# Kernel tuning notes

Measured on AMD Instinct MI355X. Metric: run time of the kernel, lower is better.

Reference implementation:

```python
import jax, jax.numpy as jnp
import numpy as np

N, E, IN_DIM, OUT_DIM, R = 50000, 800000, 128, 128, 8


def setup_inputs() -> dict:
    key = jax.random.key(0)
    k1, k2, k3, k4, k5 = jax.random.split(key, 5)
    x = jax.random.normal(k1, (N, IN_DIM), dtype=jnp.float32)
    edge_index = jax.random.randint(k2, (2, E), 0, N, dtype=jnp.int32)
    edge_type = jax.random.randint(k3, (E,), 0, R, dtype=jnp.int32)
    # Xavier-uniform-ish init for parameters
    lim_w = float(np.sqrt(6.0 / (IN_DIM + OUT_DIM)))
    weight = jax.random.uniform(k4, (R, IN_DIM, OUT_DIM), dtype=jnp.float32, minval=-lim_w, maxval=lim_w)
    self_weight = jax.random.uniform(k5, (IN_DIM, OUT_DIM), dtype=jnp.float32, minval=-lim_w, maxval=lim_w)
    return {"x": x, "weight": weight, "self_weight": self_weight,
            "edge_index": edge_index, "edge_type": edge_type}


def reference(x, weight, self_weight, edge_index, edge_type):
    n = x.shape[0]
    r = weight.shape[0]
    d_out = weight.shape[2]
    src, dst = edge_index[0], edge_index[1]
    # undirected: symmetrize edges (directed=False)
    src_all = jnp.concatenate([src, dst])          # [2E]
    dst_all = jnp.concatenate([dst, src])          # [2E]
    et_all = jnp.concatenate([edge_type, edge_type])  # [2E]
    # transform all nodes by every relation weight once: [R, N, D_out]
    xw = jnp.einsum('ni,rio->rno', x, weight)
    # gather per-edge messages already transformed by their relation's W_r
    msg = xw[et_all, src_all]                      # [2E, D_out]
    # fused (relation, dst) segment id -> per-relation scatter-add
    seg = et_all.astype(jnp.int32) * n + dst_all
    agg = jax.ops.segment_sum(msg, seg, num_segments=r * n).reshape(r, n, d_out)
    deg = jax.ops.segment_sum(jnp.ones_like(seg, dtype=x.dtype), seg,
                              num_segments=r * n).reshape(r, n)
    deg_inv = jnp.where(deg > 0, 1.0 / jnp.maximum(deg, 1.0), jnp.zeros_like(deg))
    out = jnp.sum(agg * deg_inv[..., None], axis=0)  # [N, D_out]
    out = out + x @ self_weight                       # self-loop
    return out
```

## Files before the change

kernel.cpp:

```cpp
#include <hip/hip_runtime.h>

#define NN 50000
#define EE 800000
#define RR 8
#define DD 128
#define SS (NN*RR)
#define TE (2*EE)
#define NB 782
#define NBLK 391
#define NS (NB*NBLK)
#define CONVB 6826
#define XWB 391

typedef __attribute__((ext_vector_type(8))) short bf16x8;
typedef __attribute__((ext_vector_type(4))) float f32x4;

#define DRAIN_VM do { \
    asm volatile("s_waitcnt vmcnt(0)" ::: "memory"); \
    __builtin_amdgcn_sched_barrier(0); \
  } while (0)

__device__ __forceinline__ unsigned short f2bf(float f){
  unsigned int u = __float_as_uint(f);
  u += 0x7fffu + ((u >> 16) & 1u);
  return (unsigned short)(u >> 16);
}
__device__ __forceinline__ float bf_lo(unsigned int w){ return __uint_as_float(w << 16); }
__device__ __forceinline__ float bf_hi(unsigned int w){ return __uint_as_float(w & 0xffff0000u); }

__device__ __forceinline__ void acc8(float* a, uint4 u){
  a[0] += bf_lo(u.x); a[1] += bf_hi(u.x);
  a[2] += bf_lo(u.y); a[3] += bf_hi(u.y);
  a[4] += bf_lo(u.z); a[5] += bf_hi(u.z);
  a[6] += bf_lo(u.w); a[7] += bf_hi(u.w);
}
__device__ __forceinline__ void acc8s(float* a, uint4 u, float s){
  a[0] += s*bf_lo(u.x); a[1] += s*bf_hi(u.x);
  a[2] += s*bf_lo(u.y); a[3] += s*bf_hi(u.y);
  a[4] += s*bf_lo(u.z); a[5] += s*bf_hi(u.z);
  a[6] += s*bf_lo(u.w); a[7] += s*bf_hi(u.w);
}

__device__ __forceinline__ void dir_edge(const int* ei, const int* et, int j,
                                         int& s, int& d, int& t){
  if (j < EE){ s = ei[j]; d = ei[EE + j]; t = et[j]; }
  else { int jj = j - EE; s = ei[EE + jj]; d = ei[jj]; t = et[jj]; }
}

__global__ __launch_bounds__(256) void k_histconv(
    const int* __restrict__ ei, const int* __restrict__ et,
    int* __restrict__ hist,
    const float* __restrict__ x, const float* __restrict__ w,
    const float* __restrict__ sw,
    unsigned short* __restrict__ xb, unsigned short* __restrict__ wb)
{
  __shared__ int h[NB];
  if (blockIdx.x < NBLK){
    int tid = threadIdx.x, bid = blockIdx.x;
    for (int i = tid; i < NB; i += 256) h[i] = 0;
    __syncthreads();
    int j0 = bid*4096;
    for (int k = tid; k < 4096; k += 256){
      int j = j0 + k;
      if (j < TE){
        int s, d, t; dir_edge(ei, et, j, s, d, t);
        atomicAdd(&h[d >> 6], 1);
      }
    }
    __syncthreads();
    for (int i = tid; i < NB; i += 256) hist[i*NBLK + bid] = h[i];
  } else {
    int i = (blockIdx.x - NBLK)*256 + threadIdx.x;
    const int M1 = NN*DD/4;
    if (i < M1){
      float4 v = ((const float4*)x)[i];
      ushort4 o;
      o.x = f2bf(v.x); o.y = f2bf(v.y); o.z = f2bf(v.z); o.w = f2bf(v.w);
      ((ushort4*)xb)[i] = o;
    } else {
      int j = i - M1;
      if (j < 9*DD*DD){
        int r = j >> 14; int rem = j & 16383; int n = rem >> 7; int k = rem & 127;
        float v = (r < 8) ? w[r*16384 + k*128 + n] : sw[k*128 + n];
        wb[j] = f2bf(v);
      }
    }
  }
}

__global__ __launch_bounds__(256) void k_scan1(int* __restrict__ hist,
                                               int* __restrict__ blksum){
  __shared__ int sd[256];
  int b = blockIdx.x, tid = threadIdx.x;
  int base = b*1024 + tid*4;
  int v0 = (base+0 < NS) ? hist[base+0] : 0;
  int v1 = (base+1 < NS) ? hist[base+1] : 0;
  int v2 = (base+2 < NS) ? hist[base+2] : 0;
  int v3 = (base+3 < NS) ? hist[base+3] : 0;
  int ts = v0+v1+v2+v3;
  sd[tid] = ts; __syncthreads();
  for (int o = 1; o < 256; o <<= 1){
    int t = (tid >= o) ? sd[tid-o] : 0;
    __syncthreads();
    sd[tid] += t;
    __syncthreads();
  }
  int ex = sd[tid] - ts;
  if (base+0 < NS) hist[base+0] = ex; ex += v0;
  if (base+1 < NS) hist[base+1] = ex; ex += v1;
  if (base+2 < NS) hist[base+2] = ex; ex += v2;
  if (base+3 < NS) hist[base+3] = ex;
  if (tid == 255) blksum[b] = sd[255];
}

__global__ __launch_bounds__(256) void k_scan3(int* __restrict__ hist,
                                               const int* __restrict__ blksum){
  __shared__ int sd[256];
  int b = blockIdx.x, tid = threadIdx.x;
  int chunk = b >> 2;
  int s = 0;
  if (tid < chunk)       s  = blksum[tid];
  if (tid + 256 < chunk) s += blksum[tid + 256];
  sd[tid] = s; __syncthreads();
  for (int o = 128; o > 0; o >>= 1){
    if (tid < o) sd[tid] += sd[tid + o];
    __syncthreads();
  }
  int i = b*256 + tid;
  if (i < NS) hist[i] += sd[0];
}

__global__ __launch_bounds__(256, 5) void k_partxw(
    const int* __restrict__ ei, const int* __restrict__ et,
    const int* __restrict__ S, unsigned int* __restrict__ P,
    const unsigned short* __restrict__ xb,
    const unsigned short* __restrict__ wb,
    unsigned short* __restrict__ xw)
{
  __shared__ __align__(16) unsigned short Bs[2][4096];
  if (blockIdx.x < NBLK){
    int* cur = (int*)&Bs[0][0];
    int tid = threadIdx.x, bid = blockIdx.x;
    for (int i = tid; i < NB; i += 256) cur[i] = S[i*NBLK + bid];
    __syncthreads();
    int j0 = bid*4096;
    for (int k = tid; k < 4096; k += 256){
      int j = j0 + k;
      if (j < TE){
        int s, d, t; dir_edge(ei, et, j, s, d, t);
        int b = d >> 6;
        int p = atomicAdd(&cur[b], 1);
        P[p] = (unsigned int)s | ((unsigned int)(d & 63) << 17)
             | ((unsigned int)t << 23);
      }
    }
  } else {
    const int bid  = blockIdx.x - NBLK;
    const int tid  = threadIdx.x;
    const int wave = tid >> 6, lane = tid & 63;
    const int l15  = lane & 15, quad = lane >> 4;
    const int row0 = bid * 128 + wave * 32;

    bf16x8 af[2][4];
    #pragma unroll
    for (int m = 0; m < 2; ++m){
      int gr = row0 + m*16 + l15; if (gr >= NN) gr = NN - 1;
      #pragma unroll
      for (int ks = 0; ks < 4; ++ks)
        af[m][ks] = *(const bf16x8*)(xb + (size_t)gr*DD + ks*32 + quad*8);
    }

    auto stage = [&](int rr, int qq, int bfb){
      #pragma unroll
      for (int j = 0; j < 2; ++j){
        int rowq = (wave*2 + j)*4 + (lane >> 4);
        int n = qq*32 + rowq;
        int c = lane & 15;
        const unsigned short* gp = wb + rr*16384 + n*128 + ((c ^ (n & 7)) << 3);
        __builtin_amdgcn_global_load_lds(
            (const __attribute__((address_space(1))) void*)gp,
            (__attribute__((address_space(3))) void*)((char*)&Bs[bfb][0] + (wave*2 + j)*1024),
            16, 0, 0);
      }
    };

    stage(0, 0, 0);

    #pragma unroll 1
    for (int r = 0; r < 9; ++r){
      unsigned short* xs = xw + (size_t)r * NN * DD;
      #pragma unroll
      for (int q = 0; q < 4; ++q){
        DRAIN_VM;
        __syncthreads();
        {
          int nqq = r*4 + q + 1;
          if (nqq < 36) stage(nqq >> 2, nqq & 3, (q + 1) & 1);
        }
        const char* bb = (const char*)&Bs[q & 1][0];
        #pragma unroll
        for (int lnt = 0; lnt < 2; ++lnt){
          int nt = q*2 + lnt;
          bf16x8 bf4[4];
          #pragma unroll
          for (int ks = 0; ks < 4; ++ks)
            bf4[ks] = *(const bf16x8*)(bb + (lnt*16 + l15)*256
                                          + (((ks*4 + quad) ^ (l15 & 7)) << 4));
          f32x4 C0 = (f32x4)(0.f), C1 = (f32x4)(0.f);
          #pragma unroll
          for (int ks = 0; ks < 4; ++ks){
            C0 = __builtin_amdgcn_mfma_f32_16x16x32_bf16(af[0][ks], bf4[ks], C0, 0, 0, 0);
            C1 = __builtin_amdgcn_mfma_f32_16x16x32_bf16(af[1][ks], bf4[ks], C1, 0, 0, 0);
          }
          #pragma unroll
          for (int i = 0; i < 4; ++i){
            int gr0 = row0 + quad*4 + i;
            int gr1 = row0 + 16 + quad*4 + i;
            if (gr0 < NN) xs[(size_t)gr0*DD + nt*16 + l15] = f2bf(C0[i]);
            if (gr1 < NN) xs[(size_t)gr1*DD + nt*16 + l15] = f2bf(C1[i]);
          }
        }
      }
    }
  }
}

__global__ __launch_bounds__(256) void k_build(const unsigned int* __restrict__ P,
                                               const int* __restrict__ S,
                                               int* __restrict__ esrc,
                                               int* __restrict__ offs){
  __shared__ int h[512], cu[512], sd[256];
  int tid = threadIdx.x, b = blockIdx.x;
  int pstart = S[b*NBLK];
  int pend   = (b+1 < NB) ? S[(b+1)*NBLK] : TE;
  int ne = pend - pstart;
  h[2*tid] = 0; h[2*tid+1] = 0;
  __syncthreads();
  for (int k = tid; k < ne; k += 256){
    unsigned int u = P[pstart + k];
    int lseg = (int)(((u >> 17) & 63u)*8u + (u >> 23));
    atomicAdd(&h[lseg], 1);
  }
  __syncthreads();
  int v0 = h[2*tid], v1 = h[2*tid+1];
  int ts = v0 + v1;
  sd[tid] = ts; __syncthreads();
  for (int o = 1; o < 256; o <<= 1){
    int t = (tid >= o) ? sd[tid-o] : 0;
    __syncthreads();
    sd[tid] += t;
    __syncthreads();
  }
  int ex = sd[tid] - ts;
  cu[2*tid]   = pstart + ex;
  cu[2*tid+1] = pstart + ex + v0;
  int seg0 = b*512;
  if (seg0 + 2*tid     < SS) offs[seg0 + 2*tid]     = cu[2*tid];
  if (seg0 + 2*tid + 1 < SS) offs[seg0 + 2*tid + 1] = cu[2*tid+1];
  if (b == NB-1 && tid == 0) offs[SS] = TE;
  __syncthreads();
  for (int k = tid; k < ne; k += 256){
    unsigned int u = P[pstart + k];
    int lseg = (int)(((u >> 17) & 63u)*8u + (u >> 23));
    int r = atomicAdd(&cu[lseg], 1);
    esrc[r] = (int)(u & 0x1ffffu) | (int)(((u >> 23) & 7u) << 17);
  }
}

__global__ __launch_bounds__(256, 4) void k_agg(
    const unsigned short* __restrict__ xw,
    const int* __restrict__ offs,
    const int* __restrict__ esrc,
    float* __restrict__ out)
{
  const int tid   = threadIdx.x;
  const int lane  = tid & 63;
  const int gl    = lane & 15;
  const int basel = lane & 48;
  const int d     = blockIdx.x * 16 + (tid >> 4);

  int o = 0;
  if (gl < 9) o = offs[d*8 + gl];
  int onx = __shfl(o, (basel + gl + 1) & 63);
  int cnt = onx - o;
  float scale = (gl < 8 && cnt > 0) ? 1.0f/(float)cnt : 0.0f;
  int ebase = __shfl(o, basel);
  int etot  = __shfl(o, basel + 8) - ebase;

  float a[8] = {0.f,0.f,0.f,0.f,0.f,0.f,0.f,0.f};

  int pk[8];
  #pragma unroll
  for (int s = 0; s < 8; ++s) pk[s] = (s < etot) ? esrc[ebase + s] : 0;

  for (int e = 0; e < etot; e += 8){
    uint4 U[8]; float sc[8];
    #pragma unroll
    for (int s = 0; s < 8; ++s){
      sc[s] = 0.f;
      U[s] = make_uint4(0u,0u,0u,0u);
      if (e + s < etot){
        int rel = (pk[s] >> 17) & 7;
        sc[s]   = __shfl(scale, basel + rel);
        int src = pk[s] & 0x1ffff;
        U[s] = *(const uint4*)(xw + ((size_t)rel*NN + src)*DD + gl*8);
      }
    }
    #pragma unroll
    for (int s = 0; s < 8; ++s){
      int en = e + 8 + s;
      pk[s] = (en < etot) ? esrc[ebase + en] : 0;
    }
    #pragma unroll
    for (int s = 0; s < 8; ++s) acc8s(a, U[s], sc[s]);
  }

  {
    uint4 u = *(const uint4*)(xw + ((size_t)8*NN + d)*DD + gl*8);
    acc8(a, u);
  }

  float4 v0; v0.x = a[0]; v0.y = a[1]; v0.z = a[2]; v0.w = a[3];
  float4 v1; v1.x = a[4]; v1.y = a[5]; v1.z = a[6]; v1.w = a[7];
  *(float4*)(out + (size_t)d*DD + gl*8)     = v0;
  *(float4*)(out + (size_t)d*DD + gl*8 + 4) = v1;
}

extern "C" void kernel_launch(void* const* d_in, const int* in_sizes, int n_in,
                              void* d_out, int out_size, void* d_ws, size_t ws_size,
                              hipStream_t stream){
  const float* x  = (const float*)d_in[0];
  const float* w  = (const float*)d_in[1];
  const float* sw = (const float*)d_in[2];
  const int*   ei = (const int*)d_in[3];
  const int*   et = (const int*)d_in[4];
  float* out = (float*)d_out;
  char* ws = (char*)d_ws;

  if (ws_size < (size_t)136295168) return;

  unsigned short* xb = (unsigned short*)(ws + 0);
  int*          esrc = (int*)(ws + 12800000);
  int*          offs = (int*)(ws + 19200000);
  unsigned short* wb = (unsigned short*)(ws + 20800016);
  unsigned short* xw = (unsigned short*)(ws + 21095168);

  unsigned int*    P = (unsigned int*)((char*)d_out + 0);
  int*          hist = (int*)((char*)d_out + 6400000);
  int*        blksum = (int*)((char*)d_out + 7623168);

  k_histconv<<<NBLK + CONVB, 256, 0, stream>>>(ei, et, hist, x, w, sw, xb, wb);
  k_scan1<<<(NS + 1023)/1024, 256, 0, stream>>>(hist, blksum);
  k_scan3<<<(NS + 255)/256, 256, 0, stream>>>(hist, blksum);
  k_partxw<<<NBLK + XWB, 256, 0, stream>>>(ei, et, hist, P, xb, wb, xw);
  k_build<<<NB, 256, 0, stream>>>(P, hist, esrc, offs);
  k_agg<<<NN/16, 256, 0, stream>>>(xw, offs, esrc, out);
}
```

Baseline: 229.4 us.

## Split XW GEMM across scan kernels to overlap with prefix-sum launches

Factors the bf16 MFMA XW transform into a device function and spreads its 391 row-blocks across the two scan kernels and the partition kernel, so GEMM work fills the GPU while the small, latency-bound scan kernels run. It also drops unused src/type loads from the histogram pass and widens the aggregation gather batch from 8 to 12 edges to keep more loads in flight. The cost is higher register pressure in the aggregation kernel and heavier scan kernels whose GEMM blocks may delay the dependent next launch.

```diff
diff --git a/kernel.cpp b/kernel.cpp
--- a/kernel.cpp
+++ b/kernel.cpp
@@ -10,7 +10,11 @@
 #define NBLK 391
 #define NS (NB*NBLK)
 #define CONVB 6826
-#define XWB 391
+#define SCAN1B 299
+#define SCAN3B 1195
+#define XW_A 131
+#define XW_B 130
+#define XW_C 130
 
 typedef __attribute__((ext_vector_type(8))) short bf16x8;
 typedef __attribute__((ext_vector_type(4))) float f32x4;
@@ -45,6 +49,80 @@
                                          int& s, int& d, int& t){
   if (j < EE){ s = ei[j]; d = ei[EE + j]; t = et[j]; }
   else { int jj = j - EE; s = ei[EE + jj]; d = ei[jj]; t = et[jj]; }
+}
+
+__device__ __forceinline__ void xw_block(
+    int bid, char* BsB,
+    const unsigned short* __restrict__ xb,
+    const unsigned short* __restrict__ wb,
+    unsigned short* __restrict__ xw)
+{
+  const int tid  = threadIdx.x;
+  const int wave = tid >> 6, lane = tid & 63;
+  const int l15  = lane & 15, quad = lane >> 4;
+  const int row0 = bid * 128 + wave * 32;
+
+  bf16x8 af[2][4];
+  #pragma unroll
+  for (int m = 0; m < 2; ++m){
+    int gr = row0 + m*16 + l15; if (gr >= NN) gr = NN - 1;
+    #pragma unroll
+    for (int ks = 0; ks < 4; ++ks)
+      af[m][ks] = *(const bf16x8*)(xb + (size_t)gr*DD + ks*32 + quad*8);
+  }
+
+  auto stage = [&](int rr, int qq, int bfb){
+    #pragma unroll
+    for (int j = 0; j < 2; ++j){
+      int rowq = (wave*2 + j)*4 + (lane >> 4);
+      int n = qq*32 + rowq;
+      int c = lane & 15;
+      const unsigned short* gp = wb + rr*16384 + n*128 + ((c ^ (n & 7)) << 3);
+      __builtin_amdgcn_global_load_lds(
+          (const __attribute__((address_space(1))) void*)gp,
+          (__attribute__((address_space(3))) void*)(BsB + bfb*8192 + (wave*2 + j)*1024),
+          16, 0, 0);
+    }
+  };
+
+  stage(0, 0, 0);
+
+  #pragma unroll 1
+  for (int r = 0; r < 9; ++r){
+    unsigned short* xs = xw + (size_t)r * NN * DD;
+    #pragma unroll
+    for (int q = 0; q < 4; ++q){
+      DRAIN_VM;
+      __syncthreads();
+      {
+        int nqq = r*4 + q + 1;
+        if (nqq < 36) stage(nqq >> 2, nqq & 3, (q + 1) & 1);
+      }
+      const char* bb = BsB + (q & 1)*8192;
+      #pragma unroll
+      for (int lnt = 0; lnt < 2; ++lnt){
+        int nt = q*2 + lnt;
+        bf16x8 bf4[4];
+        #pragma unroll
+        for (int ks = 0; ks < 4; ++ks)
+          bf4[ks] = *(const bf16x8*)(bb + (lnt*16 + l15)*256
+                                        + (((ks*4 + quad) ^ (l15 & 7)) << 4));
+        f32x4 C0 = (f32x4)(0.f), C1 = (f32x4)(0.f);
+        #pragma unroll
+        for (int ks = 0; ks < 4; ++ks){
+          C0 = __builtin_amdgcn_mfma_f32_16x16x32_bf16(af[0][ks], bf4[ks], C0, 0, 0, 0);
+          C1 = __builtin_amdgcn_mfma_f32_16x16x32_bf16(af[1][ks], bf4[ks], C1, 0, 0, 0);
+        }
+        #pragma unroll
+        for (int i = 0; i < 4; ++i){
+          int gr0 = row0 + quad*4 + i;
+          int gr1 = row0 + 16 + quad*4 + i;
+          if (gr0 < NN) xs[(size_t)gr0*DD + nt*16 + l15] = f2bf(C0[i]);
+          if (gr1 < NN) xs[(size_t)gr1*DD + nt*16 + l15] = f2bf(C1[i]);
+        }
+      }
+    }
+  }
 }
 
 __global__ __launch_bounds__(256) void k_histconv(
@@ -63,7 +141,7 @@
     for (int k = tid; k < 4096; k += 256){
       int j = j0 + k;
       if (j < TE){
-        int s, d, t; dir_edge(ei, et, j, s, d, t);
+        int d = (j < EE) ? ei[EE + j] : ei[j - EE];
         atomicAdd(&h[d >> 6], 1);
       }
     }
@@ -88,46 +166,64 @@
   }
 }
 
-__global__ __launch_bounds__(256) void k_scan1(int* __restrict__ hist,
-                                               int* __restrict__ blksum){
-  __shared__ int sd[256];
-  int b = blockIdx.x, tid = threadIdx.x;
-  int base = b*1024 + tid*4;
-  int v0 = (base+0 < NS) ? hist[base+0] : 0;
-  int v1 = (base+1 < NS) ? hist[base+1] : 0;
-  int v2 = (base+2 < NS) ? hist[base+2] : 0;
-  int v3 = (base+3 < NS) ? hist[base+3] : 0;
-  int ts = v0+v1+v2+v3;
-  sd[tid] = ts; __syncthreads();
-  for (int o = 1; o < 256; o <<= 1){
-    int t = (tid >= o) ? sd[tid-o] : 0;
-    __syncthreads();
-    sd[tid] += t;
-    __syncthreads();
-  }
-  int ex = sd[tid] - ts;
-  if (base+0 < NS) hist[base+0] = ex; ex += v0;
-  if (base+1 < NS) hist[base+1] = ex; ex += v1;
-  if (base+2 < NS) hist[base+2] = ex; ex += v2;
-  if (base+3 < NS) hist[base+3] = ex;
-  if (tid == 255) blksum[b] = sd[255];
-}
-
-__global__ __launch_bounds__(256) void k_scan3(int* __restrict__ hist,
-                                               const int* __restrict__ blksum){
-  __shared__ int sd[256];
-  int b = blockIdx.x, tid = threadIdx.x;
-  int chunk = b >> 2;
-  int s = 0;
-  if (tid < chunk)       s  = blksum[tid];
-  if (tid + 256 < chunk) s += blksum[tid + 256];
-  sd[tid] = s; __syncthreads();
-  for (int o = 128; o > 0; o >>= 1){
-    if (tid < o) sd[tid] += sd[tid + o];
-    __syncthreads();
-  }
-  int i = b*256 + tid;
-  if (i < NS) hist[i] += sd[0];
+__global__ __launch_bounds__(256, 5) void k_s1xw(
+    int* __restrict__ hist, int* __restrict__ blksum,
+    const unsigned short* __restrict__ xb,
+    const unsigned short* __restrict__ wb,
+    unsigned short* __restrict__ xw)
+{
+  __shared__ __align__(16) char B[16384];
+  if (blockIdx.x < SCAN1B){
+    int* sd = (int*)B;
+    int b = blockIdx.x, tid = threadIdx.x;
+    int base = b*1024 + tid*4;
+    int v0 = (base+0 < NS) ? hist[base+0] : 0;
+    int v1 = (base+1 < NS) ? hist[base+1] : 0;
+    int v2 = (base+2 < NS) ? hist[base+2] : 0;
+    int v3 = (base+3 < NS) ? hist[base+3] : 0;
+    int ts = v0+v1+v2+v3;
+    sd[tid] = ts; __syncthreads();
+    for (int o = 1; o < 256; o <<= 1){
+      int t = (tid >= o) ? sd[tid-o] : 0;
+      __syncthreads();
+      sd[tid] += t;
+      __syncthreads();
+    }
+    int ex = sd[tid] - ts;
+    if (base+0 < NS) hist[base+0] = ex; ex += v0;
+    if (base+1 < NS) hist[base+1] = ex; ex += v1;
+    if (base+2 < NS) hist[base+2] = ex; ex += v2;
+    if (base+3 < NS) hist[base+3] = ex;
+    if (tid == 255) blksum[b] = sd[255];
+  } else {
+    xw_block(blockIdx.x - SCAN1B, B, xb, wb, xw);
+  }
+}
+
+__global__ __launch_bounds__(256, 5) void k_s3xw(
+    int* __restrict__ hist, const int* __restrict__ blksum,
+    const unsigned short* __restrict__ xb,
+    const unsigned short* __restrict__ wb,
+    unsigned short* __restrict__ xw)
+{
+  __shared__ __align__(16) char B[16384];
+  if (blockIdx.x < SCAN3B){
+    int* sd = (int*)B;
+    int b = blockIdx.x, tid = threadIdx.x;
+    int chunk = b >> 2;
+    int s = 0;
+    if (tid < chunk)       s  = blksum[tid];
+    if (tid + 256 < chunk) s += blksum[tid + 256];
+    sd[tid] = s; __syncthreads();
+    for (int o = 128; o > 0; o >>= 1){
+      if (tid < o) sd[tid] += sd[tid + o];
+      __syncthreads();
+    }
+    int i = b*256 + tid;
+    if (i < NS) hist[i] += sd[0];
+  } else {
+    xw_block(blockIdx.x - SCAN3B + XW_A, B, xb, wb, xw);
+  }
 }
 
 __global__ __launch_bounds__(256, 5) void k_partxw(
@@ -137,9 +233,9 @@
     const unsigned short* __restrict__ wb,
     unsigned short* __restrict__ xw)
 {
-  __shared__ __align__(16) unsigned short Bs[2][4096];
+  __shared__ __align__(16) char B[16384];
   if (blockIdx.x < NBLK){
-    int* cur = (int*)&Bs[0][0];
+    int* cur = (int*)B;
     int tid = threadIdx.x, bid = blockIdx.x;
     for (int i = tid; i < NB; i += 256) cur[i] = S[i*NBLK + bid];
     __syncthreads();
@@ -148,80 +244,14 @@
       int j = j0 + k;
       if (j < TE){
         int s, d, t; dir_edge(ei, et, j, s, d, t);
-        int b = d >> 6;
-        int p = atomicAdd(&cur[b], 1);
+        int b2 = d >> 6;
+        int p = atomicAdd(&cur[b2], 1);
         P[p] = (unsigned int)s | ((unsigned int)(d & 63) << 17)
              | ((unsigned int)t << 23);
       }
     }
   } else {
-    const int bid  = blockIdx.x - NBLK;
-    const int tid  = threadIdx.x;
-    const int wave = tid >> 6, lane = tid & 63;
-    const int l15  = lane & 15, quad = lane >> 4;
-    const int row0 = bid * 128 + wave * 32;
-
-    bf16x8 af[2][4];
-    #pragma unroll
-    for (int m = 0; m < 2; ++m){
-      int gr = row0 + m*16 + l15; if (gr >= NN) gr = NN - 1;
-      #pragma unroll
-      for (int ks = 0; ks < 4; ++ks)
-        af[m][ks] = *(const bf16x8*)(xb + (size_t)gr*DD + ks*32 + quad*8);
-    }
-
-    auto stage = [&](int rr, int qq, int bfb){
-      #pragma unroll
-      for (int j = 0; j < 2; ++j){
-        int rowq = (wave*2 + j)*4 + (lane >> 4);
-        int n = qq*32 + rowq;
-        int c = lane & 15;
-        const unsigned short* gp = wb + rr*16384 + n*128 + ((c ^ (n & 7)) << 3);
-        __builtin_amdgcn_global_load_lds(
-            (const __attribute__((address_space(1))) void*)gp,
-            (__attribute__((address_space(3))) void*)((char*)&Bs[bfb][0] + (wave*2 + j)*1024),
-            16, 0, 0);
-      }
-    };
-
-    stage(0, 0, 0);
-
-    #pragma unroll 1
-    for (int r = 0; r < 9; ++r){
-      unsigned short* xs = xw + (size_t)r * NN * DD;
-      #pragma unroll
-      for (int q = 0; q < 4; ++q){
-        DRAIN_VM;
-        __syncthreads();
-        {
-          int nqq = r*4 + q + 1;
-          if (nqq < 36) stage(nqq >> 2, nqq & 3, (q + 1) & 1);
-        }
-        const char* bb = (const char*)&Bs[q & 1][0];
-        #pragma unroll
-        for (int lnt = 0; lnt < 2; ++lnt){
-          int nt = q*2 + lnt;
-          bf16x8 bf4[4];
-          #pragma unroll
-          for (int ks = 0; ks < 4; ++ks)
-            bf4[ks] = *(const bf16x8*)(bb + (lnt*16 + l15)*256
-                                          + (((ks*4 + quad) ^ (l15 & 7)) << 4));
-          f32x4 C0 = (f32x4)(0.f), C1 = (f32x4)(0.f);
-          #pragma unroll
-          for (int ks = 0; ks < 4; ++ks){
-            C0 = __builtin_amdgcn_mfma_f32_16x16x32_bf16(af[0][ks], bf4[ks], C0, 0, 0, 0);
-            C1 = __builtin_amdgcn_mfma_f32_16x16x32_bf16(af[1][ks], bf4[ks], C1, 0, 0, 0);
-          }
-          #pragma unroll
-          for (int i = 0; i < 4; ++i){
-            int gr0 = row0 + quad*4 + i;
-            int gr1 = row0 + 16 + quad*4 + i;
-            if (gr0 < NN) xs[(size_t)gr0*DD + nt*16 + l15] = f2bf(C0[i]);
-            if (gr1 < NN) xs[(size_t)gr1*DD + nt*16 + l15] = f2bf(C1[i]);
-          }
-        }
-      }
-    }
+    xw_block(blockIdx.x - NBLK + XW_A + XW_B, B, xb, wb, xw);
   }
 }
 
@@ -289,14 +319,14 @@
 
   float a[8] = {0.f,0.f,0.f,0.f,0.f,0.f,0.f,0.f};
 
-  int pk[8];
+  int pk[12];
   #pragma unroll
-  for (int s = 0; s < 8; ++s) pk[s] = (s < etot) ? esrc[ebase + s] : 0;
-
-  for (int e = 0; e < etot; e += 8){
-    uint4 U[8]; float sc[8];
-    #pragma unroll
-    for (int s = 0; s < 8; ++s){
+  for (int s = 0; s < 12; ++s) pk[s] = (s < etot) ? esrc[ebase + s] : 0;
+
+  for (int e = 0; e < etot; e += 12){
+    uint4 U[12]; float sc[12];
+    #pragma unroll
+    for (int s = 0; s < 12; ++s){
       sc[s] = 0.f;
       U[s] = make_uint4(0u,0u,0u,0u);
       if (e + s < etot){
@@ -307,12 +337,12 @@
       }
     }
     #pragma unroll
-    for (int s = 0; s < 8; ++s){
-      int en = e + 8 + s;
+    for (int s = 0; s < 12; ++s){
+      int en = e + 12 + s;
       pk[s] = (en < etot) ? esrc[ebase + en] : 0;
     }
     #pragma unroll
-    for (int s = 0; s < 8; ++s) acc8s(a, U[s], sc[s]);
+    for (int s = 0; s < 12; ++s) acc8s(a, U[s], sc[s]);
   }
 
   {
@@ -350,9 +380,9 @@
   int*        blksum = (int*)((char*)d_out + 7623168);
 
   k_histconv<<<NBLK + CONVB, 256, 0, stream>>>(ei, et, hist, x, w, sw, xb, wb);
-  k_scan1<<<(NS + 1023)/1024, 256, 0, stream>>>(hist, blksum);
-  k_scan3<<<(NS + 255)/256, 256, 0, stream>>>(hist, blksum);
-  k_partxw<<<NBLK + XWB, 256, 0, stream>>>(ei, et, hist, P, xb, wb, xw);
-  k_build<<<NB, 256, 0, stream>>>(P, hist, esrc, offs);
-  k_agg<<<NN/16, 256, 0, stream>>>(xw, offs, esrc, out);
-}
+  k_s1xw   <<<SCAN1B + XW_A, 256, 0, stream>>>(hist, blksum, xb, wb, xw);
+  k_s3xw   <<<SCAN3B + XW_B, 256, 0, stream>>>(hist, blksum, xb, wb, xw);
+  k_partxw <<<NBLK + XW_C, 256, 0, stream>>>(ei, et, hist, P, xb, wb, xw);
+  k_build  <<<NB, 256, 0, stream>>>(P, hist, esrc, offs);
+  k_agg    <<<NN/16, 256, 0, stream>>>(xw, offs, esrc, out);
+}
```

Result: slower. 296.1 us (+29.0%).
